# Optimization experiments

Measured on AMD Instinct MI355X. Metric: run time of the kernel, lower is better.

The kernel has to match this reference:

```python
import jax, jax.numpy as jnp
import numpy as np

N_NODES = 100000
N_EDGES = 3200000
NEG_SLOPE = 0.2  # PyG GATConv default


def _gat_conv(x, src, dst, W, a_src, a_dst, b, num_nodes):
    # x: [N, Fin]; src/dst: [E'] (self-loops already appended)
    h = x @ W                                   # [N, Fout]
    alpha_src = h @ a_src                       # [N]
    alpha_dst = h @ a_dst                       # [N]
    e = jax.nn.leaky_relu(alpha_src[src] + alpha_dst[dst], NEG_SLOPE)  # [E']
    # segment softmax over incoming edges of each destination node
    e_max = jax.ops.segment_max(e, dst, num_segments=num_nodes)
    e_exp = jnp.exp(e - e_max[dst])
    denom = jax.ops.segment_sum(e_exp, dst, num_segments=num_nodes)
    alpha = e_exp / (denom[dst] + 1e-16)        # [E']
    out = jax.ops.segment_sum(h[src] * alpha[:, None], dst, num_segments=num_nodes)
    return out + b


def setup_inputs() -> dict:
    key = jax.random.key(0)
    ks = jax.random.split(key, 10)
    x = jax.random.normal(ks[0], (N_NODES, 1), jnp.float32)
    edge_index = jax.random.randint(ks[1], (2, N_EDGES), 0, N_NODES, dtype=jnp.int64)
    s1 = 1.0  # glorot-ish scales
    return {
        "x": x,
        "edge_index": edge_index,
        "W1": jax.random.normal(ks[2], (1, 20), jnp.float32) * s1,
        "a_src1": jax.random.normal(ks[3], (20,), jnp.float32) * 0.3,
        "a_dst1": jax.random.normal(ks[4], (20,), jnp.float32) * 0.3,
        "b1": jnp.zeros((20,), jnp.float32),
        "W2": jax.random.normal(ks[5], (20, 20), jnp.float32) * (1.0 / np.sqrt(20.0)),
        "a_src2": jax.random.normal(ks[6], (20,), jnp.float32) * 0.3,
        "a_dst2": jax.random.normal(ks[7], (20,), jnp.float32) * 0.3,
        "b2": jnp.zeros((20,), jnp.float32),
        "Wl": jax.random.normal(ks[8], (20, 1), jnp.float32) * (1.0 / np.sqrt(20.0)),
        "bl": jnp.zeros((1,), jnp.float32),
    }


def reference(x, edge_index, W1, a_src1, a_dst1, b1, W2, a_src2, a_dst2, b2, Wl, bl):
    n = x.shape[0]
    loop = jnp.arange(n, dtype=edge_index.dtype)
    src = jnp.concatenate([edge_index[0], loop])  # add_self_loops=True
    dst = jnp.concatenate([edge_index[1], loop])
    h = _gat_conv(x, src, dst, W1, a_src1, a_dst1, b1, n)
    h = jax.nn.relu(h)
    h = _gat_conv(h, src, dst, W2, a_src2, a_dst2, b2, n)
    h = jax.nn.relu(h)
    return h @ Wl + bl  # [N, 1]
```

## Files before the change

kernel.cpp:

```cpp
#include <hip/hip_runtime.h>
#include <hip/hip_fp16.h>

#define FDIM 20
#define NSLOPE 0.2f
#define BSHIFT 7
#define BSIZE 128
#define BCAP 4800
#define MAXBUCK 800
#define PGRID 256
#define HSTRIDE 32
#define ABLK 512

__device__ __forceinline__ float lrelu(float v) { return v > 0.f ? v : NSLOPE * v; }

__global__ void k_init(const float* __restrict__ x, const float* __restrict__ W1,
                       const float* __restrict__ a_src, const float* __restrict__ a_dst,
                       float2* __restrict__ PX, float* __restrict__ AD,
                       int* __restrict__ gcur, int N)
{
    int i = blockIdx.x * blockDim.x + threadIdx.x;
    if (i < MAXBUCK) gcur[i] = 0;
    if (i >= N) return;
    float cs = 0.f, cd = 0.f;
#pragma unroll
    for (int f = 0; f < FDIM; ++f) { float w = W1[f]; cs += w * a_src[f]; cd += w * a_dst[f]; }
    float xv = x[i];
    PX[i] = make_float2(xv * cs, xv);
    AD[i] = xv * cd;
}

__global__ void __launch_bounds__(1024)
k_part(const int* __restrict__ ei, int E, int nbuck,
       int* __restrict__ gcur, int* __restrict__ slab)
{
    __shared__ int hist[MAXBUCK];
    __shared__ int base[MAXBUCK];
    const int chunk = (E + PGRID - 1) / PGRID;
    const int c0 = blockIdx.x * chunk;
    const int c1 = min(c0 + chunk, E);
    for (int t = threadIdx.x; t < nbuck; t += 1024) hist[t] = 0;
    __syncthreads();
    int i = c0 + 2 * threadIdx.x;
    for (; i + 1 < c1; i += 2048) {
        int2 d2 = *(const int2*)(ei + E + i);
        atomicAdd(&hist[d2.x >> BSHIFT], 1);
        atomicAdd(&hist[d2.y >> BSHIFT], 1);
    }
    if (i < c1) atomicAdd(&hist[ei[E + i] >> BSHIFT], 1);
    __syncthreads();
    for (int t = threadIdx.x; t < nbuck; t += 1024) {
        int c = hist[t];
        base[t] = c ? atomicAdd(gcur + t, c) : 0;
        hist[t] = 0;
    }
    __syncthreads();
    i = c0 + 2 * threadIdx.x;
    for (; i + 1 < c1; i += 2048) {
        int2 s2 = *(const int2*)(ei + i);
        int2 d2 = *(const int2*)(ei + E + i);
        int bA = d2.x >> BSHIFT, bB = d2.y >> BSHIFT;
        int lpA = atomicAdd(&hist[bA], 1);
        int lpB = atomicAdd(&hist[bB], 1);
        int pA = base[bA] + lpA;
        int pB = base[bB] + lpB;
        if (pA < BCAP) slab[(size_t)bA * BCAP + pA] = (s2.x << BSHIFT) | (d2.x & (BSIZE - 1));
        if (pB < BCAP) slab[(size_t)bB * BCAP + pB] = (s2.y << BSHIFT) | (d2.y & (BSIZE - 1));
    }
    if (i < c1) {
        int s = ei[i], d = ei[E + i];
        int b = d >> BSHIFT;
        int lp = atomicAdd(&hist[b], 1);
        int pos = base[b] + lp;
        if (pos < BCAP) slab[(size_t)b * BCAP + pos] = (s << BSHIFT) | (d & (BSIZE - 1));
    }
}

__device__ __forceinline__ void sort_bucket(const int* __restrict__ sp, int cnt,
                                            int* __restrict__ sedge,
                                            int* __restrict__ off,
                                            int* __restrict__ cur)
{
    const int tid = threadIdx.x;
    if (tid < BSIZE + 1) off[tid] = 0;
    __syncthreads();
    for (int i = tid; i < cnt; i += blockDim.x)
        atomicAdd(&off[(sp[i] & (BSIZE - 1)) + 1], 1);
    __syncthreads();
    for (int o = 1; o < BSIZE; o <<= 1) {
        int v = 0;
        if (tid < BSIZE && tid + 1 > o) v = off[tid + 1 - o];
        __syncthreads();
        if (tid < BSIZE) off[tid + 1] += v;
        __syncthreads();
    }
    if (tid < BSIZE) cur[tid] = off[tid];
    __syncthreads();
    for (int i = tid; i < cnt; i += blockDim.x) {
        int e = sp[i];
        int pos = atomicAdd(&cur[e & (BSIZE - 1)], 1);
        sedge[pos] = e >> BSHIFT;
    }
    __syncthreads();
}

__global__ void __launch_bounds__(ABLK)
k_agg1(const int* __restrict__ gcur, const int* __restrict__ slab,
       const float2* __restrict__ PX, const float* __restrict__ AD,
       const float* __restrict__ W1, const float* __restrict__ b1,
       const float* __restrict__ W2,
       const float* __restrict__ as2w, const float* __restrict__ ad2w,
       __half* __restrict__ H, float* __restrict__ AD2, int N)
{
    __shared__ int sedge[BCAP];
    __shared__ int off[BSIZE + 1], cur[BSIZE];
    __shared__ float sAD[BSIZE];
    __shared__ float sW1[FDIM], sb1[FDIM], sW2[FDIM * FDIM], sas[FDIM], sad[FDIM];
    const int tid = threadIdx.x;
    const int b = blockIdx.x;
    const int dbase = b << BSHIFT;
    if (tid < BSIZE) { int d = dbase + tid; sAD[tid] = (d < N) ? AD[d] : 0.f; }
    for (int t = tid; t < FDIM * FDIM; t += ABLK) sW2[t] = W2[t];
    if (tid >= 480 && tid < 480 + FDIM) {
        int k = tid - 480;
        sW1[k] = W1[k]; sb1[k] = b1[k]; sas[k] = as2w[k]; sad[k] = ad2w[k];
    }
    const int cnt = min(gcur[b], BCAP);
    sort_bucket(slab + (size_t)b * BCAP, cnt, sedge, off, cur);

    const int dl = tid >> 2, sub = tid & 3;
    const float adv = sAD[dl];
    float den = 0.f, sx = 0.f;
    const int e1 = off[dl + 1];
#pragma unroll 2
    for (int j = off[dl] + sub; j < e1; j += 4) {
        int s = sedge[j];
        float2 p = PX[s];
        float w = __expf(lrelu(p.x + adv));
        den += w; sx += w * p.y;
    }
    den += __shfl_xor(den, 1); den += __shfl_xor(den, 2);
    sx  += __shfl_xor(sx, 1);  sx  += __shfl_xor(sx, 2);
    const int d = dbase + dl;
    if (sub == 0 && d < N) {
        float2 p = PX[d];
        float w = __expf(lrelu(p.x + adv));
        den += w; sx += w * p.y;
        float sv = sx / (den + 1e-16f);
        float tk[FDIM];
#pragma unroll
        for (int k = 0; k < FDIM; ++k) {
            float tv = sv * sW1[k] + sb1[k];
            tk[k] = tv > 0.f ? tv : 0.f;
        }
        float pas = 0.f, pad = 0.f;
        __half2* hrow = (__half2*)(H + (size_t)d * HSTRIDE);
#pragma unroll
        for (int f = 0; f < FDIM; f += 2) {
            float h0 = 0.f, h1 = 0.f;
#pragma unroll
            for (int k = 0; k < FDIM; ++k) {
                h0 += tk[k] * sW2[k * FDIM + f];
                h1 += tk[k] * sW2[k * FDIM + f + 1];
            }
            hrow[f >> 1] = __halves2half2(__float2half(h0), __float2half(h1));
            pas += h0 * sas[f] + h1 * sas[f + 1];
            pad += h0 * sad[f] + h1 * sad[f + 1];
        }
        *(float*)(H + (size_t)d * HSTRIDE + FDIM) = pas;
        AD2[d] = pad;
    }
}

__global__ void __launch_bounds__(ABLK)
k_agg2(const int* __restrict__ gcur, const int* __restrict__ slab,
       const __half* __restrict__ H, const float* __restrict__ AD2,
       const float* __restrict__ b2, const float* __restrict__ Wl,
       const float* __restrict__ bl,
       float* __restrict__ out, int N)
{
    __shared__ int sedge[BCAP];
    __shared__ int off[BSIZE + 1], cur[BSIZE];
    __shared__ float sAD[BSIZE];
    __shared__ float sb2[FDIM], sWl[FDIM];
    const int tid = threadIdx.x;
    const int b = blockIdx.x;
    const int dbase = b << BSHIFT;
    if (tid < BSIZE) { int d = dbase + tid; sAD[tid] = (d < N) ? AD2[d] : 0.f; }
    if (tid >= 480 && tid < 480 + FDIM) {
        int k = tid - 480;
        sb2[k] = b2[k]; sWl[k] = Wl[k];
    }
    const int cnt = min(gcur[b], BCAP);
    sort_bucket(slab + (size_t)b * BCAP, cnt, sedge, off, cur);

    const int dl = tid >> 2, sub = tid & 3;
    const float adv = sAD[dl];
    float den = 0.f;
    float acc[FDIM];
#pragma unroll
    for (int k = 0; k < FDIM; ++k) acc[k] = 0.f;
    const int e1 = off[dl + 1];
#pragma unroll 2
    for (int j = off[dl] + sub; j < e1; j += 4) {
        int s = sedge[j];
        const uint4* rp = (const uint4*)(H + (size_t)s * HSTRIDE);
        uint4 a = rp[0];
        uint4 bb = rp[1];
        uint4 c = rp[2];
        float w = __expf(lrelu(__uint_as_float(c.z) + adv));
        den += w;
        float2 f;
        f = __half22float2(*(__half2*)&a.x);  acc[0]  += w * f.x; acc[1]  += w * f.y;
        f = __half22float2(*(__half2*)&a.y);  acc[2]  += w * f.x; acc[3]  += w * f.y;
        f = __half22float2(*(__half2*)&a.z);  acc[4]  += w * f.x; acc[5]  += w * f.y;
        f = __half22float2(*(__half2*)&a.w);  acc[6]  += w * f.x; acc[7]  += w * f.y;
        f = __half22float2(*(__half2*)&bb.x); acc[8]  += w * f.x; acc[9]  += w * f.y;
        f = __half22float2(*(__half2*)&bb.y); acc[10] += w * f.x; acc[11] += w * f.y;
        f = __half22float2(*(__half2*)&bb.z); acc[12] += w * f.x; acc[13] += w * f.y;
        f = __half22float2(*(__half2*)&bb.w); acc[14] += w * f.x; acc[15] += w * f.y;
        f = __half22float2(*(__half2*)&c.x);  acc[16] += w * f.x; acc[17] += w * f.y;
        f = __half22float2(*(__half2*)&c.y);  acc[18] += w * f.x; acc[19] += w * f.y;
    }
    den += __shfl_xor(den, 1); den += __shfl_xor(den, 2);
#pragma unroll
    for (int k = 0; k < FDIM; ++k) {
        acc[k] += __shfl_xor(acc[k], 1);
        acc[k] += __shfl_xor(acc[k], 2);
    }
    const int d = dbase + dl;
    if (sub == 0 && d < N) {
        const uint4* rp = (const uint4*)(H + (size_t)d * HSTRIDE);
        uint4 a = rp[0], bb = rp[1], c = rp[2];
        float w = __expf(lrelu(__uint_as_float(c.z) + adv));
        den += w;
        float hv[FDIM];
        float2 f;
        f = __half22float2(*(__half2*)&a.x);  hv[0]  = f.x; hv[1]  = f.y;
        f = __half22float2(*(__half2*)&a.y);  hv[2]  = f.x; hv[3]  = f.y;
        f = __half22float2(*(__half2*)&a.z);  hv[4]  = f.x; hv[5]  = f.y;
        f = __half22float2(*(__half2*)&a.w);  hv[6]  = f.x; hv[7]  = f.y;
        f = __half22float2(*(__half2*)&bb.x); hv[8]  = f.x; hv[9]  = f.y;
        f = __half22float2(*(__half2*)&bb.y); hv[10] = f.x; hv[11] = f.y;
        f = __half22float2(*(__half2*)&bb.z); hv[12] = f.x; hv[13] = f.y;
        f = __half22float2(*(__half2*)&bb.w); hv[14] = f.x; hv[15] = f.y;
        f = __half22float2(*(__half2*)&c.x);  hv[16] = f.x; hv[17] = f.y;
        f = __half22float2(*(__half2*)&c.y);  hv[18] = f.x; hv[19] = f.y;
        float inv = 1.f / (den + 1e-16f);
        float r = 0.f;
#pragma unroll
        for (int k = 0; k < FDIM; ++k) {
            float v = (acc[k] + w * hv[k]) * inv + sb2[k];
            v = v > 0.f ? v : 0.f;
            r += v * sWl[k];
        }
        out[d] = r + bl[0];
    }
}

extern "C" void kernel_launch(void* const* d_in, const int* in_sizes, int n_in,
                              void* d_out, int out_size, void* d_ws, size_t ws_size,
                              hipStream_t stream)
{
    const float* x      = (const float*)d_in[0];
    const int*   ei     = (const int*)d_in[1];
    const float* W1     = (const float*)d_in[2];
    const float* a_src1 = (const float*)d_in[3];
    const float* a_dst1 = (const float*)d_in[4];
    const float* b1     = (const float*)d_in[5];
    const float* W2     = (const float*)d_in[6];
    const float* a_src2 = (const float*)d_in[7];
    const float* a_dst2 = (const float*)d_in[8];
    const float* b2     = (const float*)d_in[9];
    const float* Wl     = (const float*)d_in[10];
    const float* bl     = (const float*)d_in[11];
    float* out = (float*)d_out;

    const int N = in_sizes[0];
    const int E = in_sizes[1] / 2;
    const int NBUCK = (N + BSIZE - 1) >> BSHIFT;

    __half* H   = (__half*)d_ws;
    float2* PX  = (float2*)(H + (size_t)N * HSTRIDE);
    float*  AD  = (float*)(PX + N);
    float*  AD2 = AD + N;
    int*  gcur  = (int*)(AD2 + N);
    int*  slab  = gcur + MAXBUCK;

    const int nb_n = (N + 255) / 256;

    k_init<<<nb_n, 256, 0, stream>>>(x, W1, a_src1, a_dst1, PX, AD, gcur, N);
    k_part<<<PGRID, 1024, 0, stream>>>(ei, E, NBUCK, gcur, slab);
    k_agg1<<<NBUCK, ABLK, 0, stream>>>(gcur, slab, PX, AD, W1, b1, W2,
                                       a_src2, a_dst2, H, AD2, N);
    k_agg2<<<NBUCK, ABLK, 0, stream>>>(gcur, slab, H, AD2, b2, Wl, bl, out, N);
}
```

Before: 196.8 us.

## Stage partitioned edges in LDS so slab writes are bucket-contiguous

The edge partition kernel now reads each edge only once, keeping entries in registers along with their local bucket rank. It then prefix-sums bucket counts in shared memory, scatters the entries into an LDS buffer sorted by bucket, and writes them to the global slab in order, so consecutive threads store to contiguous addresses. This removes the second pass over the edge list and the random global scatter writes. In exchange it uses a large amount of LDS (about 75KB), which limits occupancy, and it relies on ITMAX*1024 covering each chunk (12544 edges).

```diff
diff --git a/kernel.cpp b/kernel.cpp
--- a/kernel.cpp
+++ b/kernel.cpp
@@ -10,6 +10,8 @@
 #define PGRID 256
 #define HSTRIDE 32
 #define ABLK 512
+#define ITMAX 13
+#define CHCAP 12544
 
 __device__ __forceinline__ float lrelu(float v) { return v > 0.f ? v : NSLOPE * v; }
 
@@ -34,44 +36,67 @@
        int* __restrict__ gcur, int* __restrict__ slab)
 {
     __shared__ int hist[MAXBUCK];
-    __shared__ int base[MAXBUCK];
+    __shared__ int lofs[MAXBUCK];
+    __shared__ int gbase[MAXBUCK];
+    __shared__ int sbuf[CHCAP];
+    __shared__ unsigned short sbk[CHCAP];
+    const int tid = threadIdx.x;
     const int chunk = (E + PGRID - 1) / PGRID;
     const int c0 = blockIdx.x * chunk;
     const int c1 = min(c0 + chunk, E);
-    for (int t = threadIdx.x; t < nbuck; t += 1024) hist[t] = 0;
-    __syncthreads();
-    int i = c0 + 2 * threadIdx.x;
-    for (; i + 1 < c1; i += 2048) {
-        int2 d2 = *(const int2*)(ei + E + i);
-        atomicAdd(&hist[d2.x >> BSHIFT], 1);
-        atomicAdd(&hist[d2.y >> BSHIFT], 1);
-    }
-    if (i < c1) atomicAdd(&hist[ei[E + i] >> BSHIFT], 1);
-    __syncthreads();
-    for (int t = threadIdx.x; t < nbuck; t += 1024) {
-        int c = hist[t];
-        base[t] = c ? atomicAdd(gcur + t, c) : 0;
-        hist[t] = 0;
-    }
-    __syncthreads();
-    i = c0 + 2 * threadIdx.x;
-    for (; i + 1 < c1; i += 2048) {
-        int2 s2 = *(const int2*)(ei + i);
-        int2 d2 = *(const int2*)(ei + E + i);
-        int bA = d2.x >> BSHIFT, bB = d2.y >> BSHIFT;
-        int lpA = atomicAdd(&hist[bA], 1);
-        int lpB = atomicAdd(&hist[bB], 1);
-        int pA = base[bA] + lpA;
-        int pB = base[bB] + lpB;
-        if (pA < BCAP) slab[(size_t)bA * BCAP + pA] = (s2.x << BSHIFT) | (d2.x & (BSIZE - 1));
-        if (pB < BCAP) slab[(size_t)bB * BCAP + pB] = (s2.y << BSHIFT) | (d2.y & (BSIZE - 1));
-    }
-    if (i < c1) {
-        int s = ei[i], d = ei[E + i];
-        int b = d >> BSHIFT;
-        int lp = atomicAdd(&hist[b], 1);
-        int pos = base[b] + lp;
-        if (pos < BCAP) slab[(size_t)b * BCAP + pos] = (s << BSHIFT) | (d & (BSIZE - 1));
+    for (int t = tid; t < nbuck; t += 1024) hist[t] = 0;
+    __syncthreads();
+
+    int ent[ITMAX], meta[ITMAX];
+#pragma unroll
+    for (int it = 0; it < ITMAX; ++it) {
+        int i = c0 + tid + (it << 10);
+        meta[it] = -1;
+        if (i < c1) {
+            int s = ei[i], d = ei[E + i];
+            int b = d >> BSHIFT;
+            int lp = atomicAdd(&hist[b], 1);
+            ent[it]  = (s << BSHIFT) | (d & (BSIZE - 1));
+            meta[it] = (lp << 10) | b;
+        }
+    }
+    __syncthreads();
+
+    int myc = 0;
+    if (tid < nbuck) {
+        myc = hist[tid];
+        lofs[tid] = myc;
+        gbase[tid] = myc ? atomicAdd(gcur + tid, myc) : 0;
+    }
+    __syncthreads();
+    for (int o = 1; o < nbuck; o <<= 1) {
+        int v = 0;
+        if (tid < nbuck && tid >= o) v = lofs[tid - o];
+        __syncthreads();
+        if (tid < nbuck && tid >= o) lofs[tid] += v;
+        __syncthreads();
+    }
+    if (tid < nbuck) lofs[tid] -= myc;
+    __syncthreads();
+
+#pragma unroll
+    for (int it = 0; it < ITMAX; ++it) {
+        int m = meta[it];
+        if (m >= 0) {
+            int b  = m & 1023;
+            int lp = m >> 10;
+            int pos = lofs[b] + lp;
+            sbuf[pos] = ent[it];
+            sbk[pos]  = (unsigned short)b;
+        }
+    }
+    __syncthreads();
+
+    const int cnt = c1 - c0;
+    for (int i = tid; i < cnt; i += 1024) {
+        int b  = sbk[i];
+        int gp = gbase[b] + (i - lofs[b]);
+        if (gp < BCAP) slab[(size_t)b * BCAP + gp] = sbuf[i];
     }
 }
 
```

Result: faster. 184.4 us (-6.3%).
